# Kernel optimization log

Measured on AMD Instinct MI355X. Metric: run time of the kernel, lower is better.

## Reference

```python
import jax, jax.numpy as jnp
import numpy as np

N_QUBITS = 22


def setup_inputs() -> dict:
    n = N_QUBITS
    dim = 2 ** n
    key = jax.random.key(0)
    k1, k2, k3, k4, k5 = jax.random.split(key, 5)
    return {
        "state_real": jax.random.normal(k1, (dim,), jnp.float32),
        "state_imag": jax.random.normal(k2, (dim,), jnp.float32),
        "rabi": jax.random.uniform(k3, (1,), jnp.float32),
        "detune": jax.random.uniform(k4, (1,), jnp.float32),
        "U": jax.random.normal(k5, (n, n), jnp.float32),
        "n_qubits": n,
    }


def reference(state_real, state_imag, rabi, detune, U, n_qubits):
    """kron_sum of H_rabi (Pauli-X per qubit, weight rabi/2), diagonal detune
    (weight -detune per qubit) and diagonal pairwise interaction (triu(U,1)),
    applied to a 2**n complex state vector."""
    n = n_qubits
    dim = 2 ** n
    psi = (state_real + 1j * state_imag).astype(jnp.complex64).reshape((2,) * n)

    # parse_weights: per-qubit rabi/2 for X terms, -detune for number operators
    w_x = jnp.full((n,), rabi[0] * 0.5)
    w_d = jnp.full((n,), -detune[0])

    # sum_k (rabi/2) * X_k |psi>  : X_k flips qubit-k axis of the state tensor
    x_acc = jnp.zeros_like(psi)
    for k in range(n):  # fixed small structural loop over qubits
        x_acc = x_acc + w_x[k] * jnp.flip(psi, axis=k)

    # bit table: bits[k, b] = k-th qubit bit of basis index b (axis 0 = MSB)
    basis = jnp.arange(dim, dtype=jnp.uint32)
    shifts = jnp.arange(n - 1, -1, -1, dtype=jnp.uint32)
    bits = ((basis[None, :] >> shifts[:, None]) & 1).astype(jnp.float32)  # [n, 2**n]

    # diagonal one-body detune: sum_k w_d[k] * bit_k
    diag_one = jnp.einsum("k,kn->n", w_d, bits)
    # diagonal two-body interaction: sum_{i<j} U[i,j] * bit_i * bit_j
    Ut = jnp.triu(U, k=1)
    diag_two = jnp.sum((Ut @ bits) * bits, axis=0)

    diag = (diag_one + diag_two).reshape((2,) * n)
    out = (x_acc + diag * psi).reshape(dim)
    return jnp.stack([out.real, out.imag])  # [2, 2**n] (real, imag)
```

## Files before the change

### kernel.cpp

```cpp
#include <hip/hip_runtime.h>

#define NQ 22
#define DIM (1 << NQ)
#define TILE 2048
#define LOG_TILE 11

typedef float f32x4_t __attribute__((ext_vector_type(4)));

__global__ __launch_bounds__(256) void ryd_precompute_B(const float* __restrict__ U,
                                                        float* __restrict__ Btab) {
    int t = blockIdx.x * blockDim.x + threadIdx.x;
    __shared__ float Us[NQ * NQ];
    for (int i = threadIdx.x; i < NQ * NQ; i += blockDim.x) Us[i] = U[i];
    __syncthreads();
    float b = 0.f;
    #pragma unroll
    for (int p = 1; p <= 10; ++p) {
        if ((t >> p) & 1) {
            #pragma unroll
            for (int q = 0; q < p; ++q) {
                if ((t >> q) & 1) b += Us[(21 - p) * NQ + (21 - q)];
            }
        }
    }
    Btab[t] = b;
}

#define ACC8(a0, a1, b0, b1)                                              \
    do {                                                                  \
        ar[0] += (a0).x; ar[1] += (a0).y; ar[2] += (a0).z; ar[3] += (a0).w; \
        ar[4] += (a1).x; ar[5] += (a1).y; ar[6] += (a1).z; ar[7] += (a1).w; \
        ai[0] += (b0).x; ai[1] += (b0).y; ai[2] += (b0).z; ai[3] += (b0).w; \
        ai[4] += (b1).x; ai[5] += (b1).y; ai[6] += (b1).z; ai[7] += (b1).w; \
    } while (0)

__device__ __forceinline__ int swz(int c) { return c ^ ((c >> 3) & 1); }

__global__ __launch_bounds__(256, 4) void ryd_main(
    const float* __restrict__ sr_g, const float* __restrict__ si_g,
    const float* __restrict__ rabi, const float* __restrict__ detune,
    const float* __restrict__ U, const float* __restrict__ Btab,
    float* __restrict__ out) {
    __shared__ float4 srv[TILE / 4];
    __shared__ float4 siv[TILE / 4];
    __shared__ float AD[12];

    const int h = blockIdx.x;
    const int tid = threadIdx.x;
    const int m0 = tid << 3;
    const int base = h << LOG_TILE;

    float4 r0 = *(const float4*)(sr_g + base + m0);
    float4 r1 = *(const float4*)(sr_g + base + m0 + 4);
    float4 i0 = *(const float4*)(si_g + base + m0);
    float4 i1 = *(const float4*)(si_g + base + m0 + 4);

    float4 fr[3][2], fi[3][2];
    #pragma unroll
    for (int j = 0; j < 3; ++j) {
        const float* pa = sr_g + ((h ^ (1 << j)) << LOG_TILE) + m0;
        const float* pb = si_g + ((h ^ (1 << j)) << LOG_TILE) + m0;
        fr[j][0] = *(const float4*)pa;
        fr[j][1] = *(const float4*)(pa + 4);
        fi[j][0] = *(const float4*)pb;
        fi[j][1] = *(const float4*)(pb + 4);
    }

    float4 B0 = *(const float4*)(Btab + m0);
    float4 B1 = *(const float4*)(Btab + m0 + 4);

    srv[swz(2 * tid)]     = r0;
    srv[swz(2 * tid + 1)] = r1;
    siv[swz(2 * tid)]     = i0;
    siv[swz(2 * tid + 1)] = i1;

    if (tid < 11) {
        int q = tid;
        float d = 0.f;
        #pragma unroll
        for (int hp = 0; hp <= 10; ++hp)
            if ((h >> hp) & 1) d += U[(10 - hp) * NQ + (21 - q)];
        AD[q] = d;
    } else if (tid == 11) {
        float a = 0.f;
        #pragma unroll
        for (int hp = 1; hp <= 10; ++hp) {
            if ((h >> hp) & 1) {
                #pragma unroll
                for (int hq = 0; hq < hp; ++hq)
                    if ((h >> hq) & 1) a += U[(10 - hp) * NQ + (10 - hq)];
            }
        }
        AD[11] = a;
    }

    float pr[8]  = {r0.x, r0.y, r0.z, r0.w, r1.x, r1.y, r1.z, r1.w};
    float pi_[8] = {i0.x, i0.y, i0.z, i0.w, i1.x, i1.y, i1.z, i1.w};

    __syncthreads();

    float ar[8], ai[8];
    #pragma unroll
    for (int e = 0; e < 8; ++e) {
        ar[e] = pr[e ^ 1] + pr[e ^ 2] + pr[e ^ 4];
        ai[e] = pi_[e ^ 1] + pi_[e ^ 2] + pi_[e ^ 4];
    }

    #pragma unroll
    for (int jj = 0; jj < 8; ++jj) {
        int p = tid ^ (1 << jj);
        float4 a0 = srv[swz(2 * p)];
        float4 a1 = srv[swz(2 * p + 1)];
        float4 b0 = siv[swz(2 * p)];
        float4 b1 = siv[swz(2 * p + 1)];
        ACC8(a0, a1, b0, b1);
    }

    #pragma unroll
    for (int j = 0; j < 3; ++j) ACC8(fr[j][0], fr[j][1], fi[j][0], fi[j][1]);

    #pragma unroll
    for (int jj = 3; jj < 11; jj += 2) {
        const float* pa = sr_g + ((h ^ (1 << jj)) << LOG_TILE) + m0;
        const float* pb = si_g + ((h ^ (1 << jj)) << LOG_TILE) + m0;
        const float* pc = sr_g + ((h ^ (2 << jj)) << LOG_TILE) + m0;
        const float* pd = si_g + ((h ^ (2 << jj)) << LOG_TILE) + m0;
        float4 a0 = *(const float4*)pa;
        float4 a1 = *(const float4*)(pa + 4);
        float4 b0 = *(const float4*)pb;
        float4 b1 = *(const float4*)(pb + 4);
        float4 c0 = *(const float4*)pc;
        float4 c1 = *(const float4*)(pc + 4);
        float4 d0 = *(const float4*)pd;
        float4 d1 = *(const float4*)(pd + 4);
        ACC8(a0, a1, b0, b1);
        ACC8(c0, c1, d0, d1);
    }

    const float det = detune[0];
    const float hrabi = 0.5f * rabi[0];
    float Dq0 = AD[0] - det;
    float Dq1 = AD[1] - det;
    float Dq2 = AD[2] - det;
    float diagBase = AD[11] - det * (float)__popc((unsigned)h);
    #pragma unroll
    for (int j = 0; j < 8; ++j)
        if ((tid >> j) & 1) diagBase += AD[j + 3] - det;

    float Bv[8] = {B0.x, B0.y, B0.z, B0.w, B1.x, B1.y, B1.z, B1.w};

    float orv[8], oiv[8];
    #pragma unroll
    for (int e = 0; e < 8; ++e) {
        float d = diagBase + Bv[e];
        if (e & 1) d += Dq0;
        if (e & 2) d += Dq1;
        if (e & 4) d += Dq2;
        orv[e] = hrabi * ar[e] + d * pr[e];
        oiv[e] = hrabi * ai[e] + d * pi_[e];
    }

    f32x4_t o0 = {orv[0], orv[1], orv[2], orv[3]};
    f32x4_t o1 = {orv[4], orv[5], orv[6], orv[7]};
    f32x4_t o2 = {oiv[0], oiv[1], oiv[2], oiv[3]};
    f32x4_t o3 = {oiv[4], oiv[5], oiv[6], oiv[7]};
    __builtin_nontemporal_store(o0, (f32x4_t*)(out + base + m0));
    __builtin_nontemporal_store(o1, (f32x4_t*)(out + base + m0 + 4));
    __builtin_nontemporal_store(o2, (f32x4_t*)(out + DIM + base + m0));
    __builtin_nontemporal_store(o3, (f32x4_t*)(out + DIM + base + m0 + 4));
}

extern "C" void kernel_launch(void* const* d_in, const int* in_sizes, int n_in,
                              void* d_out, int out_size, void* d_ws, size_t ws_size,
                              hipStream_t stream) {
    const float* state_real = (const float*)d_in[0];
    const float* state_imag = (const float*)d_in[1];
    const float* rabi       = (const float*)d_in[2];
    const float* detune     = (const float*)d_in[3];
    const float* U          = (const float*)d_in[4];
    float* Btab = (float*)d_ws;
    float* out  = (float*)d_out;

    ryd_precompute_B<<<TILE / 256, 256, 0, stream>>>(U, Btab);
    ryd_main<<<DIM / TILE, 256, 0, stream>>>(state_real, state_imag, rabi, detune,
                                             U, Btab, out);
}
```

Before: 123.1 us.

## Split flip accumulation into row kernel and LDS-transposed column kernel

The main kernel now handles only the low 11 qubit flips (within a 2048-element tile) plus the diagonal term. A new kernel loads a 2048x16 column slab per block into shared memory and accumulates the 11 high-qubit flips, adding them to the output via read-modify-write. This replaces eleven strided global re-reads of the state per element with roughly two passes, at the cost of an extra output round-trip and a second launch. The column kernel uses a large shared buffer, limiting occupancy, and issues short 64-byte strided loads.

```diff
diff --git a/kernel.cpp b/kernel.cpp
--- a/kernel.cpp
+++ b/kernel.cpp
@@ -36,7 +36,7 @@
 
 __device__ __forceinline__ int swz(int c) { return c ^ ((c >> 3) & 1); }
 
-__global__ __launch_bounds__(256, 4) void ryd_main(
+__global__ __launch_bounds__(256) void ryd_rows(
     const float* __restrict__ sr_g, const float* __restrict__ si_g,
     const float* __restrict__ rabi, const float* __restrict__ detune,
     const float* __restrict__ U, const float* __restrict__ Btab,
@@ -54,17 +54,6 @@
     float4 r1 = *(const float4*)(sr_g + base + m0 + 4);
     float4 i0 = *(const float4*)(si_g + base + m0);
     float4 i1 = *(const float4*)(si_g + base + m0 + 4);
-
-    float4 fr[3][2], fi[3][2];
-    #pragma unroll
-    for (int j = 0; j < 3; ++j) {
-        const float* pa = sr_g + ((h ^ (1 << j)) << LOG_TILE) + m0;
-        const float* pb = si_g + ((h ^ (1 << j)) << LOG_TILE) + m0;
-        fr[j][0] = *(const float4*)pa;
-        fr[j][1] = *(const float4*)(pa + 4);
-        fi[j][0] = *(const float4*)pb;
-        fi[j][1] = *(const float4*)(pb + 4);
-    }
 
     float4 B0 = *(const float4*)(Btab + m0);
     float4 B1 = *(const float4*)(Btab + m0 + 4);
@@ -116,27 +105,6 @@
         ACC8(a0, a1, b0, b1);
     }
 
-    #pragma unroll
-    for (int j = 0; j < 3; ++j) ACC8(fr[j][0], fr[j][1], fi[j][0], fi[j][1]);
-
-    #pragma unroll
-    for (int jj = 3; jj < 11; jj += 2) {
-        const float* pa = sr_g + ((h ^ (1 << jj)) << LOG_TILE) + m0;
-        const float* pb = si_g + ((h ^ (1 << jj)) << LOG_TILE) + m0;
-        const float* pc = sr_g + ((h ^ (2 << jj)) << LOG_TILE) + m0;
-        const float* pd = si_g + ((h ^ (2 << jj)) << LOG_TILE) + m0;
-        float4 a0 = *(const float4*)pa;
-        float4 a1 = *(const float4*)(pa + 4);
-        float4 b0 = *(const float4*)pb;
-        float4 b1 = *(const float4*)(pb + 4);
-        float4 c0 = *(const float4*)pc;
-        float4 c1 = *(const float4*)(pc + 4);
-        float4 d0 = *(const float4*)pd;
-        float4 d1 = *(const float4*)(pd + 4);
-        ACC8(a0, a1, b0, b1);
-        ACC8(c0, c1, d0, d1);
-    }
-
     const float det = detune[0];
     const float hrabi = 0.5f * rabi[0];
     float Dq0 = AD[0] - det;
@@ -160,14 +128,46 @@
         oiv[e] = hrabi * ai[e] + d * pi_[e];
     }
 
-    f32x4_t o0 = {orv[0], orv[1], orv[2], orv[3]};
-    f32x4_t o1 = {orv[4], orv[5], orv[6], orv[7]};
-    f32x4_t o2 = {oiv[0], oiv[1], oiv[2], oiv[3]};
-    f32x4_t o3 = {oiv[4], oiv[5], oiv[6], oiv[7]};
-    __builtin_nontemporal_store(o0, (f32x4_t*)(out + base + m0));
-    __builtin_nontemporal_store(o1, (f32x4_t*)(out + base + m0 + 4));
-    __builtin_nontemporal_store(o2, (f32x4_t*)(out + DIM + base + m0));
-    __builtin_nontemporal_store(o3, (f32x4_t*)(out + DIM + base + m0 + 4));
+    *(float4*)(out + base + m0)           = make_float4(orv[0], orv[1], orv[2], orv[3]);
+    *(float4*)(out + base + m0 + 4)       = make_float4(orv[4], orv[5], orv[6], orv[7]);
+    *(float4*)(out + DIM + base + m0)     = make_float4(oiv[0], oiv[1], oiv[2], oiv[3]);
+    *(float4*)(out + DIM + base + m0 + 4) = make_float4(oiv[4], oiv[5], oiv[6], oiv[7]);
+}
+
+__global__ __launch_bounds__(1024, 4) void ryd_cols(
+    const float* __restrict__ sr_g, const float* __restrict__ si_g,
+    const float* __restrict__ rabi, float* __restrict__ out) {
+    __shared__ f32x4_t L[TILE * 4];
+
+    const int b = blockIdx.x;
+    const int A = b & 1;
+    const int C0 = (b >> 1) << 4;
+    const float* __restrict__ src = A ? si_g : sr_g;
+    float* __restrict__ dst = out + (A ? DIM : 0);
+    const int t = threadIdx.x;
+    const float hrabi = 0.5f * rabi[0];
+
+    #pragma unroll
+    for (int k = 0; k < 8; ++k) {
+        int n = t + (k << 10);
+        int r = n >> 2, cv = n & 3;
+        L[(r << 2) + cv] = *(const f32x4_t*)(src + (r << 11) + C0 + (cv << 2));
+    }
+    __syncthreads();
+
+    #pragma unroll
+    for (int k = 0; k < 8; ++k) {
+        int n = t + (k << 10);
+        int r = n >> 2, cv = n & 3;
+        f32x4_t acc = L[((r ^ 1) << 2) + cv];
+        #pragma unroll
+        for (int j = 1; j < 11; ++j)
+            acc += L[(((r ^ (1 << j)) << 2)) + cv];
+        float* o = dst + (r << 11) + C0 + (cv << 2);
+        f32x4_t cur = __builtin_nontemporal_load((const f32x4_t*)o);
+        f32x4_t res = cur + acc * hrabi;
+        __builtin_nontemporal_store(res, (f32x4_t*)o);
+    }
 }
 
 extern "C" void kernel_launch(void* const* d_in, const int* in_sizes, int n_in,
@@ -182,6 +182,7 @@
     float* out  = (float*)d_out;
 
     ryd_precompute_B<<<TILE / 256, 256, 0, stream>>>(U, Btab);
-    ryd_main<<<DIM / TILE, 256, 0, stream>>>(state_real, state_imag, rabi, detune,
+    ryd_rows<<<DIM / TILE, 256, 0, stream>>>(state_real, state_imag, rabi, detune,
                                              U, Btab, out);
+    ryd_cols<<<256, 1024, 0, stream>>>(state_real, state_imag, rabi, out);
 }
```

Result: slower. 132.4 us (+7.6%).
